# Kernel optimization log

Hardware: AMD Instinct MI355X
Metric: run time of the kernel (lower is better)

Reference implementation:

```python
import jax, jax.numpy as jnp
import numpy as np

N = 50000   # num_semes / nodes
E = 800000  # edges
R = 8       # num_relations
D = 128     # embed_dim
H = 128     # rgcn_hidden_dim
EPS = 1e-5


def layer_norm(x, g, b):
    mu = jnp.mean(x, axis=-1, keepdims=True)
    var = jnp.mean(jnp.square(x - mu), axis=-1, keepdims=True)
    return (x - mu) * jax.lax.rsqrt(var + EPS) * g + b


def rgcn_conv(x, W, root, bias, edge_index, edge_type, num_relations):
    # PyG RGCNConv (default aggr='mean', root weight + bias):
    # out[i] = sum_r mean_{j in N_r(i)} x[j] @ W_r + x[i] @ root + bias
    src, dst = edge_index[0], edge_index[1]
    n = x.shape[0]
    seg = dst * num_relations + edge_type  # combined (node, relation) segment id
    msgs = x[src]  # [E, d_in]
    agg = jax.ops.segment_sum(msgs, seg, num_segments=n * num_relations)
    agg = agg.reshape(n, num_relations, -1)  # [N, R, d_in]
    cnt = jax.ops.segment_sum(jnp.ones((msgs.shape[0],), dtype=x.dtype), seg,
                              num_segments=n * num_relations)
    cnt = cnt.reshape(n, num_relations, 1)
    mean = agg / jnp.maximum(cnt, 1.0)  # zero where no edges of that relation
    out = jnp.einsum('nrd,rdo->no', mean, W) + x @ root + bias
    return out


def setup_inputs() -> dict:
    key = jax.random.key(0)
    ks = jax.random.split(key, 20)
    f32 = jnp.float32
    def glorot(k, shape):
        fan = shape[-2]
        return jax.random.normal(k, shape, dtype=f32) / np.float32(np.sqrt(fan))
    return {
        'node_ids':  jax.random.randint(ks[0], (N,), 0, N),
        'edge_index': jax.random.randint(ks[1], (2, E), 0, N),
        'edge_type': jax.random.randint(ks[2], (E,), 0, R),
        'emb':   jax.random.normal(ks[3], (N, D), dtype=f32) * 0.02,
        'W1':    glorot(ks[4], (R, D, H)),
        'root1': glorot(ks[5], (D, H)),
        'b1':    jnp.zeros((H,), f32),
        'g1':    jnp.ones((H,), f32),
        'be1':   jnp.zeros((H,), f32),
        'W2':    glorot(ks[6], (R, H, H)),
        'root2': glorot(ks[7], (H, H)),
        'b2':    jnp.zeros((H,), f32),
        'g2':    jnp.ones((H,), f32),
        'be2':   jnp.zeros((H,), f32),
        'W3':    glorot(ks[8], (R, H, D)),
        'root3': glorot(ks[9], (H, D)),
        'b3':    jnp.zeros((D,), f32),
    }


def reference(node_ids, edge_index, edge_type, emb,
              W1, root1, b1, g1, be1,
              W2, root2, b2, g2, be2,
              W3, root3, b3):
    x = emb[node_ids]                                  # sememe embedding lookup
    x = rgcn_conv(x, W1, root1, b1, edge_index, edge_type, R)
    x = jax.nn.relu(layer_norm(x, g1, be1))            # dropout: eval mode (identity)
    x = rgcn_conv(x, W2, root2, b2, edge_index, edge_type, R)
    x = jax.nn.relu(layer_norm(x, g2, be2))
    x = rgcn_conv(x, W3, root3, b3, edge_index, edge_type, R)
    return x
```

## Files before the change

kernel.cpp:

```cpp
#include <hip/hip_runtime.h>
#include <hip/hip_bf16.h>
#include <stdint.h>


#define N_NODES 50000
#define N_EDGES 800000
#define R_REL 8
#define NSEG (N_NODES * R_REL)

typedef __bf16 bf16_8 __attribute__((ext_vector_type(8)));
typedef float floatx4 __attribute__((ext_vector_type(4)));
typedef unsigned short ushort8 __attribute__((ext_vector_type(8)));

static __device__ __forceinline__ float bf2f(unsigned short v) {
    unsigned u = ((unsigned)v) << 16;
    return __builtin_bit_cast(float, u);
}
static __device__ __forceinline__ unsigned short f2bf(float f) {
    unsigned u = __builtin_bit_cast(unsigned, f);
    u += 0x7FFFu + ((u >> 16) & 1u);
    return (unsigned short)(u >> 16);
}

__global__ void k_detect(const unsigned* __restrict__ g1, unsigned* __restrict__ flag) {
    if (threadIdx.x == 0 && blockIdx.x == 0)
        flag[0] = (g1[0] == 0x3F803F80u) ? 1u : 0u;
}


__global__ void k_zero(unsigned* __restrict__ p, int n_words) {
    int i = blockIdx.x * blockDim.x + threadIdx.x;
    int stride = gridDim.x * blockDim.x;
    for (; i < n_words; i += stride) p[i] = 0u;
}

__global__ void k_count(const int* __restrict__ ei, const int* __restrict__ et,
                        unsigned* __restrict__ cnt_nt, unsigned* __restrict__ rank) {
    int e = blockIdx.x * 256 + threadIdx.x;
    if (e >= N_EDGES) return;
    int dst = ei[N_EDGES + e];
    int t = et[e];
    rank[e] = atomicAdd(&cnt_nt[dst * R_REL + t], 1u);
}

#define SCAN_B 1024
#define SCAN_NB ((NSEG + SCAN_B - 1) / SCAN_B)

__global__ void k_scan1(const unsigned* __restrict__ deg, unsigned* __restrict__ escan,
                        unsigned* __restrict__ bsum) {
    __shared__ unsigned wsum[16];
    int tid = threadIdx.x;
    int lane = tid & 63, wid = tid >> 6;
    int i = blockIdx.x * SCAN_B + tid;
    unsigned v = (i < NSEG) ? deg[i] : 0u;
    unsigned incl = v;
#pragma unroll
    for (int d = 1; d < 64; d <<= 1) {
        unsigned t = __shfl_up(incl, d, 64);
        if (lane >= d) incl += t;
    }
    if (lane == 63) wsum[wid] = incl;
    __syncthreads();
    if (wid == 0 && lane < 16) {
        unsigned w = wsum[lane];
#pragma unroll
        for (int d = 1; d < 16; d <<= 1) {
            unsigned t = __shfl_up(w, d, 64);
            if (lane >= d) w += t;
        }
        wsum[lane] = w;
    }
    __syncthreads();
    unsigned woff = (wid == 0) ? 0u : wsum[wid - 1];
    if (i < NSEG) escan[i] = woff + incl - v;
    if (tid == 0) bsum[blockIdx.x] = wsum[15];
}

__global__ void k_scan2(const unsigned* __restrict__ bsum, unsigned* __restrict__ boff,
                        unsigned* __restrict__ offs) {
    __shared__ unsigned ws[8];
    int tid = threadIdx.x;
    int lane = tid & 63, w = tid >> 6;
    unsigned b = (tid < SCAN_NB) ? bsum[tid] : 0u;
    unsigned incl = b;
#pragma unroll
    for (int d = 1; d < 64; d <<= 1) {
        unsigned t = __shfl_up(incl, d, 64);
        if (lane >= d) incl += t;
    }
    if (lane == 63) ws[w] = incl;
    __syncthreads();
    unsigned wpre = 0;
    for (int i = 0; i < w; ++i) wpre += ws[i];
    if (tid < SCAN_NB) boff[tid] = wpre + incl - b;
    if (tid == 511) offs[NSEG] = wpre + incl;
}

__global__ void k_scan3(const unsigned* __restrict__ escan, const unsigned* __restrict__ boff,
                        unsigned* __restrict__ offs) {
    int i = blockIdx.x * SCAN_B + threadIdx.x;
    if (i < NSEG) offs[i] = escan[i] + boff[blockIdx.x];
}

__global__ void k_fill(const int* __restrict__ ei, const int* __restrict__ et,
                       const unsigned* __restrict__ offs, const unsigned* __restrict__ rank,
                       unsigned* __restrict__ csr) {
    int e = blockIdx.x * 256 + threadIdx.x;
    if (e >= N_EDGES) return;
    int src = ei[e];
    int dst = ei[N_EDGES + e];
    int t = et[e];
    csr[offs[dst * R_REL + t] + rank[e]] = (unsigned)src;
}

__global__ void k_transw(const unsigned* __restrict__ flag,
                         const void* __restrict__ W1, const void* __restrict__ r1,
                         const void* __restrict__ W2, const void* __restrict__ r2,
                         const void* __restrict__ W3, const void* __restrict__ r3,
                         unsigned short* __restrict__ WT) {
    int idx = blockIdx.x * 256 + threadIdx.x;
    if (idx >= 27 * 128 * 128) return;
    int is_bf = (int)flag[0];
    int m = idx >> 14;
    int r = idx & 16383;
    int o = r >> 7, d = r & 127;
    int l = m / 9, j = m % 9;
    const void* W = (l == 0) ? W1 : (l == 1) ? W2 : W3;
    const void* rt = (l == 0) ? r1 : (l == 1) ? r2 : r3;
    size_t eoff = (size_t)d * 128 + o;
    unsigned short v;
    if (j == 0) {
        v = is_bf ? ((const unsigned short*)rt)[eoff]
                  : f2bf(((const float*)rt)[eoff]);
    } else {
        size_t base = (size_t)(j - 1) * 16384;
        v = is_bf ? ((const unsigned short*)W)[base + eoff]
                  : f2bf(((const float*)W)[base + eoff]);
    }
    WT[idx] = v;
}

__global__ void k_gather(const unsigned* __restrict__ flag,
                         const int* __restrict__ ids, const void* __restrict__ emb,
                         unsigned short* __restrict__ x) {
    int c = blockIdx.x * 256 + threadIdx.x;
    if (c >= N_NODES * 32) return;
    int is_bf = (int)flag[0];
    int row = c >> 5, k = (c & 31) << 2;
    size_t s = (size_t)ids[row] * 128 + k;
    if (is_bf) {
        *(uint2*)&x[(size_t)row * 128 + k] = *(const uint2*)((const unsigned short*)emb + s);
    } else {
        const float4 f = *(const float4*)((const float*)emb + s);
        unsigned p0 = (unsigned)f2bf(f.x) | ((unsigned)f2bf(f.y) << 16);
        unsigned p1 = (unsigned)f2bf(f.z) | ((unsigned)f2bf(f.w) << 16);
        uint2 u; u.x = p0; u.y = p1;
        *(uint2*)&x[(size_t)row * 128 + k] = u;
    }
}

__global__ void k_cvtvec(const unsigned* __restrict__ flag,
                         const void* p0, const void* p1, const void* p2,
                         const void* p3, const void* p4, const void* p5,
                         const void* p6, float* __restrict__ vecs) {
    int v = blockIdx.x, i = threadIdx.x;
    const void* p = (v == 0) ? p0 : (v == 1) ? p1 : (v == 2) ? p2 :
                    (v == 3) ? p3 : (v == 4) ? p4 : (v == 5) ? p5 : p6;
    float f = flag[0] ? bf2f(((const unsigned short*)p)[i]) : ((const float*)p)[i];
    vecs[v * 128 + i] = f;
}

__global__ __launch_bounds__(256) void k_aggmean(
    const unsigned short* __restrict__ X,
    const unsigned* __restrict__ offs,
    const unsigned* __restrict__ csr,
    unsigned short* __restrict__ xc)
{
    int n = blockIdx.x * 4 + (threadIdx.x >> 6);
    int lane = threadIdx.x & 63;
    int c0 = lane * 2;
    unsigned ov = (lane < 9) ? offs[n * R_REL + lane] : 0u;
    unsigned eb = __shfl(ov, 0, 64);
    unsigned ee = __shfl(ov, 8, 64);
    float sx[8], sy[8];
#pragma unroll
    for (int r = 0; r < 8; ++r) { sx[r] = 0.f; sy[r] = 0.f; }

    for (unsigned base = eb; base < ee; base += 64) {
        unsigned cnt = min(64u, ee - base);
        unsigned pk = (lane < cnt) ? csr[base + lane] : 0u;
        unsigned top = base + cnt;
#pragma unroll
        for (int r = 0; r < 8; ++r) {
            unsigned lo = __shfl(ov, r, 64);
            unsigned hi = __shfl(ov, r + 1, 64);
            lo = lo > base ? lo : base;
            hi = hi < top ? hi : top;
            int j = (int)(lo - base);
            int jend = (hi > lo) ? (int)(hi - base) : j;
            for (; j + 2 <= jend; j += 2) {
                unsigned p0 = __shfl(pk, j, 64);
                unsigned p1 = __shfl(pk, j + 1, 64);
                unsigned v0 = *(const unsigned*)&X[(size_t)p0 * 128 + c0];
                unsigned v1 = *(const unsigned*)&X[(size_t)p1 * 128 + c0];
                sx[r] += bf2f((unsigned short)(v0 & 0xFFFFu)) + bf2f((unsigned short)(v1 & 0xFFFFu));
                sy[r] += bf2f((unsigned short)(v0 >> 16)) + bf2f((unsigned short)(v1 >> 16));
            }
            if (j < jend) {
                unsigned p = __shfl(pk, j, 64);
                unsigned v = *(const unsigned*)&X[(size_t)p * 128 + c0];
                sx[r] += bf2f((unsigned short)(v & 0xFFFFu));
                sy[r] += bf2f((unsigned short)(v >> 16));
            }
        }
    }

#pragma unroll
    for (int r = 0; r < 8; ++r) {
        unsigned lo = __shfl(ov, r, 64);
        unsigned hi = __shfl(ov, r + 1, 64);
        unsigned c = hi - lo;
        float inv = c ? (1.f / (float)c) : 0.f;
        unsigned out = (unsigned)f2bf(sx[r] * inv) | ((unsigned)f2bf(sy[r] * inv) << 16);
        *(unsigned*)&xc[(size_t)n * 1024 + r * 128 + c0] = out;
    }
}


#define LDT 72

__global__ __launch_bounds__(256) void k_gemm(
    const unsigned short* __restrict__ X,
    const unsigned short* __restrict__ XC,
    const unsigned short* __restrict__ WTL,
    const float* __restrict__ bias,
    const float* __restrict__ g,
    const float* __restrict__ be,
    void* __restrict__ outp,
    int do_ln,
    const unsigned* __restrict__ flag)
{
    __shared__ unsigned short As[128 * LDT];
    __shared__ unsigned short Bs[128 * LDT];
    int tid = threadIdx.x;
    int m0 = blockIdx.x * 128;
    int lane = tid & 63, wave = tid >> 6;
    int wm = wave * 32;
    int rr = lane & 15, qq = lane >> 4;

    floatx4 acc[2][8];
#pragma unroll
    for (int i = 0; i < 2; i++)
#pragma unroll
        for (int j = 0; j < 8; j++) acc[i][j] = (floatx4){0.f, 0.f, 0.f, 0.f};

    for (int ks = 0; ks < 18; ++ks) {
        int k0 = ks * 64;
        const unsigned short* bsrc = WTL + (size_t)(k0 >> 7) * 16384 + (k0 & 127);
#pragma unroll
        for (int i = 0; i < 4; ++i) {
            int c = tid + i * 256;
            int row = c >> 3;
            int kc = (c & 7) << 3;
            int grow = m0 + row;
            if (grow >= N_NODES) grow = N_NODES - 1;
            const unsigned short* asrc = (k0 < 128)
                ? &X[(size_t)grow * 128 + k0 + kc]
                : &XC[(size_t)grow * 1024 + (k0 - 128) + kc];
            *(ushort8*)&As[row * LDT + kc] = *(const ushort8*)asrc;
            *(ushort8*)&Bs[row * LDT + kc] = *(const ushort8*)&bsrc[row * 128 + kc];
        }
        __syncthreads();
#pragma unroll
        for (int kk = 0; kk < 2; ++kk) {
            int kb = kk * 32 + qq * 8;
            bf16_8 a[2], b[8];
#pragma unroll
            for (int i = 0; i < 2; i++)
                a[i] = __builtin_bit_cast(bf16_8, *(const ushort8*)&As[(wm + i * 16 + rr) * LDT + kb]);
#pragma unroll
            for (int j = 0; j < 8; j++)
                b[j] = __builtin_bit_cast(bf16_8, *(const ushort8*)&Bs[(j * 16 + rr) * LDT + kb]);
#pragma unroll
            for (int i = 0; i < 2; i++)
#pragma unroll
                for (int j = 0; j < 8; j++)
                    acc[i][j] = __builtin_amdgcn_mfma_f32_16x16x32_bf16(a[i], b[j], acc[i][j], 0, 0, 0);
        }
        __syncthreads();
    }

    float bs_[8];
#pragma unroll
    for (int j = 0; j < 8; ++j) bs_[j] = bias[j * 16 + rr];

    if (do_ln) {
        float g_[8], be_[8];
#pragma unroll
        for (int j = 0; j < 8; ++j) { g_[j] = g[j * 16 + rr]; be_[j] = be[j * 16 + rr]; }
        unsigned short* O = (unsigned short*)outp;
#pragma unroll
        for (int i = 0; i < 2; ++i) {
#pragma unroll
            for (int p = 0; p < 4; ++p) {
                int row = m0 + wm + i * 16 + qq * 4 + p;
                float v[8]; float s1 = 0.f, s2 = 0.f;
#pragma unroll
                for (int j = 0; j < 8; ++j) {
                    v[j] = acc[i][j][p] + bs_[j];
                    s1 += v[j]; s2 += v[j] * v[j];
                }
#pragma unroll
                for (int d = 1; d < 16; d <<= 1) {
                    s1 += __shfl_xor(s1, d, 64);
                    s2 += __shfl_xor(s2, d, 64);
                }
                float mu = s1 * (1.f / 128.f);
                float var = s2 * (1.f / 128.f) - mu * mu;
                float rs = rsqrtf(var + 1e-5f);
                if (row < N_NODES) {
#pragma unroll
                    for (int j = 0; j < 8; ++j) {
                        float t = (v[j] - mu) * rs * g_[j] + be_[j];
                        t = t > 0.f ? t : 0.f;
                        O[(size_t)row * 128 + j * 16 + rr] = f2bf(t);
                    }
                }
            }
        }
    } else {
        int is_bf = (int)flag[0];
#pragma unroll
        for (int i = 0; i < 2; ++i) {
#pragma unroll
            for (int p = 0; p < 4; ++p) {
                int row = m0 + wm + i * 16 + qq * 4 + p;
                if (row < N_NODES) {
                    if (is_bf) {
                        unsigned short* O = (unsigned short*)outp;
#pragma unroll
                        for (int j = 0; j < 8; ++j)
                            O[(size_t)row * 128 + j * 16 + rr] = f2bf(acc[i][j][p] + bs_[j]);
                    } else {
                        float* O = (float*)outp;
#pragma unroll
                        for (int j = 0; j < 8; ++j)
                            O[(size_t)row * 128 + j * 16 + rr] = acc[i][j][p] + bs_[j];
                    }
                }
            }
        }
    }
}


extern "C" void kernel_launch(void* const* d_in, const int* in_sizes, int n_in,
                              void* d_out, int out_size, void* d_ws, size_t ws_size,
                              hipStream_t stream) {
    const int* node_ids = (const int*)d_in[0];
    const int* ei = (const int*)d_in[1];
    const int* et = (const int*)d_in[2];
    const void* emb = d_in[3];
    const void* W1 = d_in[4];
    const void* r1 = d_in[5];
    const void* b1 = d_in[6];
    const void* g1 = d_in[7];
    const void* be1 = d_in[8];
    const void* W2 = d_in[9];
    const void* r2 = d_in[10];
    const void* b2 = d_in[11];
    const void* g2 = d_in[12];
    const void* be2 = d_in[13];
    const void* W3 = d_in[14];
    const void* r3 = d_in[15];
    const void* b3 = d_in[16];

    char* ws = (char*)d_ws;
    size_t off = 0;
    auto alloc = [&](size_t bytes) -> char* {
        char* p = ws + off;
        off = (off + bytes + 1023) & ~(size_t)1023;
        return p;
    };
    unsigned* cnt_nt = (unsigned*)alloc((size_t)NSEG * 4);
    size_t zero_end = off;
    unsigned* rank   = (unsigned*)alloc((size_t)N_EDGES * 4);
    unsigned* offs   = (unsigned*)alloc((size_t)(NSEG + 1) * 4);
    unsigned* escan  = (unsigned*)alloc((size_t)NSEG * 4);
    unsigned* bsum   = (unsigned*)alloc((size_t)SCAN_NB * 4);
    unsigned* boff   = (unsigned*)alloc((size_t)SCAN_NB * 4);
    unsigned* csr    = (unsigned*)alloc((size_t)N_EDGES * 4);
    unsigned short* WT = (unsigned short*)alloc((size_t)27 * 16384 * 2);
    float* vecs      = (float*)alloc((size_t)7 * 128 * 4);
    unsigned* flag   = (unsigned*)alloc(64);
    unsigned short* h  = (unsigned short*)alloc((size_t)N_NODES * 128 * 2);
    unsigned short* xc = (unsigned short*)alloc((size_t)N_NODES * 1024 * 2);
    (void)ws_size; (void)in_sizes; (void)n_in; (void)out_size;

    k_detect<<<1, 64, 0, stream>>>((const unsigned*)g1, flag);
    k_zero<<<512, 256, 0, stream>>>((unsigned*)ws, (int)(zero_end / 4));
    k_count<<<(N_EDGES + 255) / 256, 256, 0, stream>>>(ei, et, cnt_nt, rank);
    k_scan1<<<SCAN_NB, SCAN_B, 0, stream>>>(cnt_nt, escan, bsum);
    k_scan2<<<1, 512, 0, stream>>>(bsum, boff, offs);
    k_scan3<<<SCAN_NB, SCAN_B, 0, stream>>>(escan, boff, offs);
    k_fill<<<(N_EDGES + 255) / 256, 256, 0, stream>>>(ei, et, offs, rank, csr);
    k_transw<<<(27 * 16384 + 255) / 256, 256, 0, stream>>>(flag, W1, r1, W2, r2, W3, r3, WT);
    k_cvtvec<<<7, 128, 0, stream>>>(flag, b1, g1, be1, b2, g2, be2, b3, vecs);
    k_gather<<<(N_NODES * 32 + 255) / 256, 256, 0, stream>>>(flag, node_ids, emb, h);

    dim3 ggrid((N_NODES + 127) / 128);

    k_aggmean<<<N_NODES / 4, 256, 0, stream>>>(h, offs, csr, xc);
    k_gemm<<<ggrid, 256, 0, stream>>>(h, xc, WT + (size_t)0 * 9 * 16384,
                                      vecs + 0 * 128, vecs + 1 * 128, vecs + 2 * 128, h, 1, flag);
    k_aggmean<<<N_NODES / 4, 256, 0, stream>>>(h, offs, csr, xc);
    k_gemm<<<ggrid, 256, 0, stream>>>(h, xc, WT + (size_t)1 * 9 * 16384,
                                      vecs + 3 * 128, vecs + 4 * 128, vecs + 5 * 128, h, 1, flag);
    k_aggmean<<<N_NODES / 4, 256, 0, stream>>>(h, offs, csr, xc);
    k_gemm<<<ggrid, 256, 0, stream>>>(h, xc, WT + (size_t)2 * 9 * 16384,
                                      vecs + 6 * 128, vecs + 1 * 128, vecs + 2 * 128, d_out, 0, flag);
}
```

Baseline: 513.6 us.

## Fuse mean aggregation into the RGCN GEMM with relation-major CSR

Replaces the separate aggregation kernel and GEMM with one fused kernel per layer. The CSR is reordered to relation-major, with the destination packed into the high 16 bits of each entry. Each block of 64 nodes computes its per-relation means straight into swizzled LDS tiles, double-buffered so the MFMA on one relation overlaps the gather for the next. This removes the large [N,8,128] intermediate write and read, and ping-pong buffers replace the in-place h update. The cost is more LDS per block, serial run-length aggregation inside each wave, and a 16-bit packing of src/dst that depends on N being below 65536.

```diff
diff --git a/kernel.cpp b/kernel.cpp
--- a/kernel.cpp
+++ b/kernel.cpp
@@ -10,7 +10,6 @@
 
 typedef __bf16 bf16_8 __attribute__((ext_vector_type(8)));
 typedef float floatx4 __attribute__((ext_vector_type(4)));
-typedef unsigned short ushort8 __attribute__((ext_vector_type(8)));
 
 static __device__ __forceinline__ float bf2f(unsigned short v) {
     unsigned u = ((unsigned)v) << 16;
@@ -21,6 +20,9 @@
     u += 0x7FFFu + ((u >> 16) & 1u);
     return (unsigned short)(u >> 16);
 }
+static __device__ __forceinline__ int sw(int row, int b) {
+    return (row << 8) + (b ^ ((row & 7) << 4));
+}
 
 __global__ void k_detect(const unsigned* __restrict__ g1, unsigned* __restrict__ flag) {
     if (threadIdx.x == 0 && blockIdx.x == 0)
@@ -35,12 +37,12 @@
 }
 
 __global__ void k_count(const int* __restrict__ ei, const int* __restrict__ et,
-                        unsigned* __restrict__ cnt_nt, unsigned* __restrict__ rank) {
+                        unsigned* __restrict__ cnt, unsigned* __restrict__ rank) {
     int e = blockIdx.x * 256 + threadIdx.x;
     if (e >= N_EDGES) return;
     int dst = ei[N_EDGES + e];
     int t = et[e];
-    rank[e] = atomicAdd(&cnt_nt[dst * R_REL + t], 1u);
+    rank[e] = atomicAdd(&cnt[t * N_NODES + dst], 1u);
 }
 
 #define SCAN_B 1024
@@ -110,7 +112,7 @@
     int src = ei[e];
     int dst = ei[N_EDGES + e];
     int t = et[e];
-    csr[offs[dst * R_REL + t] + rank[e]] = (unsigned)src;
+    csr[offs[(size_t)t * N_NODES + dst] + rank[e]] = (unsigned)src | ((unsigned)dst << 16);
 }
 
 __global__ void k_transw(const unsigned* __restrict__ flag,
@@ -170,68 +172,11 @@
     vecs[v * 128 + i] = f;
 }
 
-__global__ __launch_bounds__(256) void k_aggmean(
+
+__global__ __launch_bounds__(256) void k_fused(
     const unsigned short* __restrict__ X,
     const unsigned* __restrict__ offs,
     const unsigned* __restrict__ csr,
-    unsigned short* __restrict__ xc)
-{
-    int n = blockIdx.x * 4 + (threadIdx.x >> 6);
-    int lane = threadIdx.x & 63;
-    int c0 = lane * 2;
-    unsigned ov = (lane < 9) ? offs[n * R_REL + lane] : 0u;
-    unsigned eb = __shfl(ov, 0, 64);
-    unsigned ee = __shfl(ov, 8, 64);
-    float sx[8], sy[8];
-#pragma unroll
-    for (int r = 0; r < 8; ++r) { sx[r] = 0.f; sy[r] = 0.f; }
-
-    for (unsigned base = eb; base < ee; base += 64) {
-        unsigned cnt = min(64u, ee - base);
-        unsigned pk = (lane < cnt) ? csr[base + lane] : 0u;
-        unsigned top = base + cnt;
-#pragma unroll
-        for (int r = 0; r < 8; ++r) {
-            unsigned lo = __shfl(ov, r, 64);
-            unsigned hi = __shfl(ov, r + 1, 64);
-            lo = lo > base ? lo : base;
-            hi = hi < top ? hi : top;
-            int j = (int)(lo - base);
-            int jend = (hi > lo) ? (int)(hi - base) : j;
-            for (; j + 2 <= jend; j += 2) {
-                unsigned p0 = __shfl(pk, j, 64);
-                unsigned p1 = __shfl(pk, j + 1, 64);
-                unsigned v0 = *(const unsigned*)&X[(size_t)p0 * 128 + c0];
-                unsigned v1 = *(const unsigned*)&X[(size_t)p1 * 128 + c0];
-                sx[r] += bf2f((unsigned short)(v0 & 0xFFFFu)) + bf2f((unsigned short)(v1 & 0xFFFFu));
-                sy[r] += bf2f((unsigned short)(v0 >> 16)) + bf2f((unsigned short)(v1 >> 16));
-            }
-            if (j < jend) {
-                unsigned p = __shfl(pk, j, 64);
-                unsigned v = *(const unsigned*)&X[(size_t)p * 128 + c0];
-                sx[r] += bf2f((unsigned short)(v & 0xFFFFu));
-                sy[r] += bf2f((unsigned short)(v >> 16));
-            }
-        }
-    }
-
-#pragma unroll
-    for (int r = 0; r < 8; ++r) {
-        unsigned lo = __shfl(ov, r, 64);
-        unsigned hi = __shfl(ov, r + 1, 64);
-        unsigned c = hi - lo;
-        float inv = c ? (1.f / (float)c) : 0.f;
-        unsigned out = (unsigned)f2bf(sx[r] * inv) | ((unsigned)f2bf(sy[r] * inv) << 16);
-        *(unsigned*)&xc[(size_t)n * 1024 + r * 128 + c0] = out;
-    }
-}
-
-
-#define LDT 72
-
-__global__ __launch_bounds__(256) void k_gemm(
-    const unsigned short* __restrict__ X,
-    const unsigned short* __restrict__ XC,
     const unsigned short* __restrict__ WTL,
     const float* __restrict__ bias,
     const float* __restrict__ g,
@@ -240,90 +185,188 @@
     int do_ln,
     const unsigned* __restrict__ flag)
 {
-    __shared__ unsigned short As[128 * LDT];
-    __shared__ unsigned short Bs[128 * LDT];
+    __shared__ __align__(16) unsigned char lds[65536];
+    char* AbA = (char*)lds;
+    char* AbB = (char*)lds + 16384;
+    char* Bsm = (char*)lds + 32768;
+
     int tid = threadIdx.x;
-    int m0 = blockIdx.x * 128;
-    int lane = tid & 63, wave = tid >> 6;
-    int wm = wave * 32;
+    int m0 = blockIdx.x * 64;
+    int lane = tid & 63, wv = tid >> 6;
     int rr = lane & 15, qq = lane >> 4;
-
-    floatx4 acc[2][8];
+    int wr = wv >> 1, wc = wv & 1;
+    int c0 = lane * 2;
+
+    floatx4 acc[2][4];
 #pragma unroll
     for (int i = 0; i < 2; i++)
 #pragma unroll
-        for (int j = 0; j < 8; j++) acc[i][j] = (floatx4){0.f, 0.f, 0.f, 0.f};
-
-    for (int ks = 0; ks < 18; ++ks) {
-        int k0 = ks * 64;
-        const unsigned short* bsrc = WTL + (size_t)(k0 >> 7) * 16384 + (k0 & 127);
-#pragma unroll
-        for (int i = 0; i < 4; ++i) {
+        for (int j = 0; j < 4; j++) acc[i][j] = (floatx4){0.f, 0.f, 0.f, 0.f};
+
+#pragma unroll
+    for (int i = 0; i < 4; ++i) {
+        int c = tid + i * 256;
+        int row = c >> 4, kg = c & 15;
+        int grow = m0 + row; if (grow > N_NODES - 1) grow = N_NODES - 1;
+        uint4 v = *(const uint4*)&X[(size_t)grow * 128 + kg * 8];
+        *(uint4*)(AbA + sw(row, kg * 16)) = v;
+    }
+#pragma unroll
+    for (int i = 0; i < 8; ++i) {
+        int c = tid + i * 256;
+        uint4 v = *(const uint4*)&WTL[(size_t)c * 8];
+        *(uint4*)(Bsm + sw(c >> 4, (c & 15) * 16)) = v;
+    }
+    __syncthreads();
+
+    auto mfma_phase = [&](const char* Abc) {
+#pragma unroll
+        for (int kk = 0; kk < 4; ++kk) {
+            int ko = kk * 64 + qq * 16;
+            bf16_8 a[2], b[4];
+#pragma unroll
+            for (int i = 0; i < 2; ++i) {
+                int row = wr * 32 + i * 16 + rr;
+                a[i] = *(const bf16_8*)(Abc + sw(row, ko));
+            }
+#pragma unroll
+            for (int j = 0; j < 4; ++j) {
+                int row = wc * 64 + j * 16 + rr;
+                b[j] = *(const bf16_8*)(Bsm + sw(row, ko));
+            }
+#pragma unroll
+            for (int i = 0; i < 2; ++i)
+#pragma unroll
+                for (int j = 0; j < 4; ++j)
+                    acc[i][j] = __builtin_amdgcn_mfma_f32_16x16x32_bf16(a[i], b[j], acc[i][j], 0, 0, 0);
+        }
+    };
+
+    for (int p = 0; p < 8; ++p) {
+        char* Abc = (p & 1) ? AbB : AbA;
+        char* AbN = (p & 1) ? AbA : AbB;
+
+        uint4 breg[8];
+        const unsigned short* WTn = WTL + (size_t)(p + 1) * 16384;
+#pragma unroll
+        for (int i = 0; i < 8; ++i)
+            breg[i] = *(const uint4*)&WTn[(size_t)(tid + i * 256) * 8];
+
+        {
+            int nb = wv * 16;
+#pragma unroll
+            for (int t = 0; t < 16; ++t)
+                *(unsigned*)(AbN + sw(nb + t, lane * 4)) = 0u;
+            int gb = m0 + nb;
+            int i0 = gb < N_NODES ? gb : N_NODES;
+            int i1 = (gb + 16) < N_NODES ? (gb + 16) : N_NODES;
+            unsigned lo = offs[(size_t)p * N_NODES + i0];
+            unsigned hi = offs[(size_t)p * N_NODES + i1];
+            float ax = 0.f, ay = 0.f;
+            int cur = -1, rl = 0;
+            auto flushf = [&]() {
+                if (cur >= 0) {
+                    float inv = 1.0f / (float)rl;
+                    unsigned o = (unsigned)f2bf(ax * inv) | ((unsigned)f2bf(ay * inv) << 16);
+                    *(unsigned*)(AbN + sw(cur - m0, lane * 4)) = o;
+                }
+            };
+            auto procf = [&](unsigned q, unsigned v) {
+                int d = (int)(q >> 16);
+                if (d != cur) { flushf(); cur = d; ax = 0.f; ay = 0.f; rl = 0; }
+                ax += bf2f((unsigned short)(v & 0xFFFFu));
+                ay += bf2f((unsigned short)(v >> 16));
+                ++rl;
+            };
+            for (unsigned bs = lo; bs < hi; bs += 64) {
+                int cnt = (int)((hi - bs) < 64u ? (hi - bs) : 64u);
+                unsigned pk = (lane < cnt) ? csr[bs + lane] : 0u;
+                int j = 0;
+                for (; j + 4 <= cnt; j += 4) {
+                    unsigned q0 = __shfl(pk, j, 64);
+                    unsigned q1 = __shfl(pk, j + 1, 64);
+                    unsigned q2 = __shfl(pk, j + 2, 64);
+                    unsigned q3 = __shfl(pk, j + 3, 64);
+                    unsigned v0 = *(const unsigned*)&X[(size_t)(q0 & 0xFFFFu) * 128 + c0];
+                    unsigned v1 = *(const unsigned*)&X[(size_t)(q1 & 0xFFFFu) * 128 + c0];
+                    unsigned v2 = *(const unsigned*)&X[(size_t)(q2 & 0xFFFFu) * 128 + c0];
+                    unsigned v3 = *(const unsigned*)&X[(size_t)(q3 & 0xFFFFu) * 128 + c0];
+                    procf(q0, v0); procf(q1, v1); procf(q2, v2); procf(q3, v3);
+                }
+                for (; j < cnt; ++j) {
+                    unsigned q = __shfl(pk, j, 64);
+                    unsigned v = *(const unsigned*)&X[(size_t)(q & 0xFFFFu) * 128 + c0];
+                    procf(q, v);
+                }
+            }
+            flushf();
+        }
+
+        mfma_phase(Abc);
+
+        __syncthreads();
+#pragma unroll
+        for (int i = 0; i < 8; ++i) {
             int c = tid + i * 256;
-            int row = c >> 3;
-            int kc = (c & 7) << 3;
-            int grow = m0 + row;
-            if (grow >= N_NODES) grow = N_NODES - 1;
-            const unsigned short* asrc = (k0 < 128)
-                ? &X[(size_t)grow * 128 + k0 + kc]
-                : &XC[(size_t)grow * 1024 + (k0 - 128) + kc];
-            *(ushort8*)&As[row * LDT + kc] = *(const ushort8*)asrc;
-            *(ushort8*)&Bs[row * LDT + kc] = *(const ushort8*)&bsrc[row * 128 + kc];
+            *(uint4*)(Bsm + sw(c >> 4, (c & 15) * 16)) = breg[i];
         }
         __syncthreads();
-#pragma unroll
-        for (int kk = 0; kk < 2; ++kk) {
-            int kb = kk * 32 + qq * 8;
-            bf16_8 a[2], b[8];
-#pragma unroll
-            for (int i = 0; i < 2; i++)
-                a[i] = __builtin_bit_cast(bf16_8, *(const ushort8*)&As[(wm + i * 16 + rr) * LDT + kb]);
-#pragma unroll
-            for (int j = 0; j < 8; j++)
-                b[j] = __builtin_bit_cast(bf16_8, *(const ushort8*)&Bs[(j * 16 + rr) * LDT + kb]);
-#pragma unroll
-            for (int i = 0; i < 2; i++)
-#pragma unroll
-                for (int j = 0; j < 8; j++)
-                    acc[i][j] = __builtin_amdgcn_mfma_f32_16x16x32_bf16(a[i], b[j], acc[i][j], 0, 0, 0);
-        }
-        __syncthreads();
-    }
-
-    float bs_[8];
-#pragma unroll
-    for (int j = 0; j < 8; ++j) bs_[j] = bias[j * 16 + rr];
+    }
+    mfma_phase(AbA);
+
+    float b_[4];
+#pragma unroll
+    for (int j = 0; j < 4; ++j) b_[j] = bias[wc * 64 + j * 16 + rr];
 
     if (do_ln) {
-        float g_[8], be_[8];
-#pragma unroll
-        for (int j = 0; j < 8; ++j) { g_[j] = g[j * 16 + rr]; be_[j] = be[j * 16 + rr]; }
-        unsigned short* O = (unsigned short*)outp;
+        float g_[4], be_[4];
+#pragma unroll
+        for (int j = 0; j < 4; ++j) {
+            int col = wc * 64 + j * 16 + rr;
+            g_[j] = g[col]; be_[j] = be[col];
+        }
+        float* scr = (float*)AbB;
 #pragma unroll
         for (int i = 0; i < 2; ++i) {
 #pragma unroll
-            for (int p = 0; p < 4; ++p) {
-                int row = m0 + wm + i * 16 + qq * 4 + p;
-                float v[8]; float s1 = 0.f, s2 = 0.f;
-#pragma unroll
-                for (int j = 0; j < 8; ++j) {
-                    v[j] = acc[i][j][p] + bs_[j];
-                    s1 += v[j]; s2 += v[j] * v[j];
+            for (int pp = 0; pp < 4; ++pp) {
+                int row = wr * 32 + i * 16 + qq * 4 + pp;
+                float s1 = 0.f, s2 = 0.f;
+#pragma unroll
+                for (int j = 0; j < 4; ++j) {
+                    float v = acc[i][j][pp] + b_[j];
+                    acc[i][j][pp] = v;
+                    s1 += v; s2 += v * v;
                 }
 #pragma unroll
                 for (int d = 1; d < 16; d <<= 1) {
                     s1 += __shfl_xor(s1, d, 64);
                     s2 += __shfl_xor(s2, d, 64);
                 }
-                float mu = s1 * (1.f / 128.f);
-                float var = s2 * (1.f / 128.f) - mu * mu;
+                if (rr == 0) {
+                    scr[row * 4 + wc * 2] = s1;
+                    scr[row * 4 + wc * 2 + 1] = s2;
+                }
+            }
+        }
+        __syncthreads();
+        unsigned short* O = (unsigned short*)outp;
+#pragma unroll
+        for (int i = 0; i < 2; ++i) {
+#pragma unroll
+            for (int pp = 0; pp < 4; ++pp) {
+                int row = wr * 32 + i * 16 + qq * 4 + pp;
+                float t1 = scr[row * 4] + scr[row * 4 + 2];
+                float t2 = scr[row * 4 + 1] + scr[row * 4 + 3];
+                float mu = t1 * (1.f / 128.f);
+                float var = t2 * (1.f / 128.f) - mu * mu;
                 float rs = rsqrtf(var + 1e-5f);
-                if (row < N_NODES) {
-#pragma unroll
-                    for (int j = 0; j < 8; ++j) {
-                        float t = (v[j] - mu) * rs * g_[j] + be_[j];
+                if (m0 + row < N_NODES) {
+#pragma unroll
+                    for (int j = 0; j < 4; ++j) {
+                        float t = (acc[i][j][pp] - mu) * rs * g_[j] + be_[j];
                         t = t > 0.f ? t : 0.f;
-                        O[(size_t)row * 128 + j * 16 + rr] = f2bf(t);
+                        O[(size_t)(m0 + row) * 128 + wc * 64 + j * 16 + rr] = f2bf(t);
                     }
                 }
             }
@@ -333,19 +376,21 @@
 #pragma unroll
         for (int i = 0; i < 2; ++i) {
 #pragma unroll
-            for (int p = 0; p < 4; ++p) {
-                int row = m0 + wm + i * 16 + qq * 4 + p;
-                if (row < N_NODES) {
+            for (int pp = 0; pp < 4; ++pp) {
+                int row = wr * 32 + i * 16 + qq * 4 + pp;
+                if (m0 + row < N_NODES) {
                     if (is_bf) {
                         unsigned short* O = (unsigned short*)outp;
 #pragma unroll
-                        for (int j = 0; j < 8; ++j)
-                            O[(size_t)row * 128 + j * 16 + rr] = f2bf(acc[i][j][p] + bs_[j]);
+                        for (int j = 0; j < 4; ++j)
+                            O[(size_t)(m0 + row) * 128 + wc * 64 + j * 16 + rr] =
+                                f2bf(acc[i][j][pp] + b_[j]);
                     } else {
                         float* O = (float*)outp;
 #pragma unroll
-                        for (int j = 0; j < 8; ++j)
-                            O[(size_t)row * 128 + j * 16 + rr] = acc[i][j][p] + bs_[j];
+                        for (int j = 0; j < 4; ++j)
+                            O[(size_t)(m0 + row) * 128 + wc * 64 + j * 16 + rr] =
+                                acc[i][j][pp] + b_[j];
                     }
                 }
             }
@@ -382,7 +427,7 @@
         off = (off + bytes + 1023) & ~(size_t)1023;
         return p;
     };
-    unsigned* cnt_nt = (unsigned*)alloc((size_t)NSEG * 4);
+    unsigned* cnt    = (unsigned*)alloc((size_t)NSEG * 4);
     size_t zero_end = off;
     unsigned* rank   = (unsigned*)alloc((size_t)N_EDGES * 4);
     unsigned* offs   = (unsigned*)alloc((size_t)(NSEG + 1) * 4);
@@ -393,30 +438,30 @@
     unsigned short* WT = (unsigned short*)alloc((size_t)27 * 16384 * 2);
     float* vecs      = (float*)alloc((size_t)7 * 128 * 4);
     unsigned* flag   = (unsigned*)alloc(64);
-    unsigned short* h  = (unsigned short*)alloc((size_t)N_NODES * 128 * 2);
-    unsigned short* xc = (unsigned short*)alloc((size_t)N_NODES * 1024 * 2);
+    unsigned short* h0 = (unsigned short*)alloc((size_t)N_NODES * 128 * 2);
+    unsigned short* h1 = (unsigned short*)alloc((size_t)N_NODES * 128 * 2);
     (void)ws_size; (void)in_sizes; (void)n_in; (void)out_size;
 
     k_detect<<<1, 64, 0, stream>>>((const unsigned*)g1, flag);
     k_zero<<<512, 256, 0, stream>>>((unsigned*)ws, (int)(zero_end / 4));
-    k_count<<<(N_EDGES + 255) / 256, 256, 0, stream>>>(ei, et, cnt_nt, rank);
-    k_scan1<<<SCAN_NB, SCAN_B, 0, stream>>>(cnt_nt, escan, bsum);
+    k_count<<<(N_EDGES + 255) / 256, 256, 0, stream>>>(ei, et, cnt, rank);
+    k_scan1<<<SCAN_NB, SCAN_B, 0, stream>>>(cnt, escan, bsum);
     k_scan2<<<1, 512, 0, stream>>>(bsum, boff, offs);
     k_scan3<<<SCAN_NB, SCAN_B, 0, stream>>>(escan, boff, offs);
     k_fill<<<(N_EDGES + 255) / 256, 256, 0, stream>>>(ei, et, offs, rank, csr);
     k_transw<<<(27 * 16384 + 255) / 256, 256, 0, stream>>>(flag, W1, r1, W2, r2, W3, r3, WT);
     k_cvtvec<<<7, 128, 0, stream>>>(flag, b1, g1, be1, b2, g2, be2, b3, vecs);
-    k_gather<<<(N_NODES * 32 + 255) / 256, 256, 0, stream>>>(flag, node_ids, emb, h);
-
-    dim3 ggrid((N_NODES + 127) / 128);
-
-    k_aggmean<<<N_NODES / 4, 256, 0, stream>>>(h, offs, csr, xc);
-    k_gemm<<<ggrid, 256, 0, stream>>>(h, xc, WT + (size_t)0 * 9 * 16384,
-                                      vecs + 0 * 128, vecs + 1 * 128, vecs + 2 * 128, h, 1, flag);
-    k_aggmean<<<N_NODES / 4, 256, 0, stream>>>(h, offs, csr, xc);
-    k_gemm<<<ggrid, 256, 0, stream>>>(h, xc, WT + (size_t)1 * 9 * 16384,
-                                      vecs + 3 * 128, vecs + 4 * 128, vecs + 5 * 128, h, 1, flag);
-    k_aggmean<<<N_NODES / 4, 256, 0, stream>>>(h, offs, csr, xc);
-    k_gemm<<<ggrid, 256, 0, stream>>>(h, xc, WT + (size_t)2 * 9 * 16384,
-                                      vecs + 6 * 128, vecs + 1 * 128, vecs + 2 * 128, d_out, 0, flag);
-}
+    k_gather<<<(N_NODES * 32 + 255) / 256, 256, 0, stream>>>(flag, node_ids, emb, h0);
+
+    dim3 fgrid((N_NODES + 63) / 64);
+
+    k_fused<<<fgrid, 256, 0, stream>>>(h0, offs, csr, WT + (size_t)0 * 9 * 16384,
+                                       vecs + 0 * 128, vecs + 1 * 128, vecs + 2 * 128,
+                                       h1, 1, flag);
+    k_fused<<<fgrid, 256, 0, stream>>>(h1, offs, csr, WT + (size_t)1 * 9 * 16384,
+                                       vecs + 3 * 128, vecs + 4 * 128, vecs + 5 * 128,
+                                       h0, 1, flag);
+    k_fused<<<fgrid, 256, 0, stream>>>(h0, offs, csr, WT + (size_t)2 * 9 * 16384,
+                                       vecs + 6 * 128, vecs + 1 * 128, vecs + 2 * 128,
+                                       d_out, 0, flag);
+}
```

After: 712.0 us. 1.39x slower.
